# Kernel tuning notes

Hardware: AMD Instinct MI355X
Metric: run time of the kernel (lower is better)

Reference implementation:

```python
import math
import jax, jax.numpy as jnp
import numpy as np


def setup_inputs() -> dict:
    key = jax.random.key(0)
    k1, k2 = jax.random.split(key)
    x = jax.random.normal(k1, (16, 256, 4096), dtype=jnp.float32)          # [B, D, T]
    codebooks = jax.random.normal(k2, (8, 1024, 256), dtype=jnp.float32)   # [n_q, bins, D]
    return {"x": x, "codebooks": codebooks, "sample_rate": 24000}


def _rvq(xt, codebooks):
    """Residual VQ on channels-last input xt: [B, T, D]. codebooks: [n_q, bins, D]."""
    n_q = codebooks.shape[0]
    residual = xt
    quant_out = jnp.zeros_like(xt)
    codes = []
    losses = []
    for i in range(n_q):
        cb = codebooks[i]                                   # [bins, D]
        # squared euclidean distance: ||r||^2 - 2 r.e + ||e||^2  -> [B, T, bins]
        dist = (jnp.sum(residual * residual, axis=-1, keepdims=True)
                - 2.0 * jnp.einsum("btd,kd->btk", residual, cb)
                + jnp.sum(cb * cb, axis=-1))
        idx = jnp.argmin(dist, axis=-1)                     # [B, T]
        q = cb[idx]                                         # gather -> [B, T, D]
        # straight-through estimator
        q_st = residual + jax.lax.stop_gradient(q - residual)
        # commitment loss: mse(stop_grad(quantize), residual)
        losses.append(jnp.mean((jax.lax.stop_gradient(q_st) - residual) ** 2))
        residual = residual - q_st
        quant_out = quant_out + q_st
        codes.append(idx)
    codes = jnp.stack(codes)                                # [n_q, B, T]
    commit_loss = jnp.stack(losses)                         # [n_q]
    return quant_out, codes, commit_loss


def reference(x, codebooks, sample_rate):
    n_q, bins, _ = codebooks.shape
    bw_per_q = math.log2(bins) * sample_rate / 1000.0
    xt = jnp.transpose(x, (0, 2, 1))                        # [B, T, D]
    quant_out, codes, commit_loss = _rvq(xt, codebooks)
    quantized = jnp.transpose(quant_out, (0, 2, 1))         # [B, D, T]
    bw = jnp.asarray(n_q * bw_per_q, dtype=x.dtype)
    return quantized, codes, bw, jnp.mean(commit_loss)
```

## Files before the change

### kernel.cpp

```cpp
#include <hip/hip_runtime.h>

#define B 16
#define D 256
#define T 4096
#define NQ 8
#define BINS 1024
#define EPS 0.008f

#define OFF_C  ((size_t)B * D * T)
#define OFF_BW (OFF_C + (size_t)NQ * B * T)
#define OFF_L  (OFF_BW + 1)

typedef __attribute__((ext_vector_type(8))) short short8v;
typedef __attribute__((ext_vector_type(4))) float float4v;

#define BUF0   0
#define BUF1   16384
#define BUF2   32768
#define RESF   0
#define IDXS   16448
#define FLAGS  16704
#define G1L    16960
#define RSTG   17216
#define REDW   18240
#define REDIW  18272
#define NORMS  49152
#define SMTOT  53248

#define STAGE16(gp, loff) \
  __builtin_amdgcn_global_load_lds( \
      (const __attribute__((address_space(1))) unsigned int*)(gp), \
      (__attribute__((address_space(3))) unsigned int*)(smc + (loff)), 16, 0, 0)

__device__ __forceinline__ unsigned short f2bf(float f) {
    unsigned u = __float_as_uint(f);
    unsigned r = (u + 0x7fffu + ((u >> 16) & 1u)) >> 16;
    return (unsigned short)r;
}
__device__ __forceinline__ float bf2f(unsigned short h) {
    return __uint_as_float(((unsigned)h) << 16);
}

__global__ __launch_bounds__(256) void cbnorm_kernel(const float* __restrict__ cb,
                                                     double* __restrict__ cbn,
                                                     float* __restrict__ cbnf)
{
    const int wave = threadIdx.x >> 6;
    const int lane = threadIdx.x & 63;
    const int bin = blockIdx.x * 4 + wave;
    const float4 v = *(const float4*)&cb[(size_t)bin * D + lane * 4];
    double a = (double)v.x * v.x + (double)v.y * v.y
             + (double)v.z * v.z + (double)v.w * v.w;
    #pragma unroll
    for (int off = 32; off >= 1; off >>= 1)
        a += __shfl_xor(a, off, 64);
    if (lane == 0) { cbn[bin] = a; cbnf[bin] = (float)a; }
}

__global__ __launch_bounds__(256) void prep_bfrag(const float* __restrict__ cb,
                                                  unsigned short* __restrict__ bfh,
                                                  unsigned short* __restrict__ bfl)
{
    const int c = blockIdx.x * 4 + (threadIdx.x >> 6);
    const int lane = threadIdx.x & 63;
    const int q = c >> 9, ntg = (c >> 3) & 63, ks = c & 7;
    const float* src = cb + ((size_t)q * BINS + ntg * 16 + (lane & 15)) * D
                         + ks * 32 + (lane >> 4) * 8;
    short8v h, l;
    #pragma unroll
    for (int j = 0; j < 8; ++j) {
        const float v = src[j];
        const unsigned short hh = f2bf(v);
        h[j] = (short)hh;
        l[j] = (short)f2bf(v - bf2f(hh));
    }
    const size_t off = ((size_t)c * 64 + lane) * 8;
    *(short8v*)(bfh + off) = h;
    *(short8v*)(bfl + off) = l;
}

__global__ __launch_bounds__(256, 3) void rvq_scan(
    const float* __restrict__ rsrc, float* __restrict__ rdst,
    const float* __restrict__ cb,
    const double* __restrict__ cbn, const float* __restrict__ cbnf,
    const unsigned short* __restrict__ bfh, const unsigned short* __restrict__ bfl,
    float* __restrict__ out, double* __restrict__ lpart, int q)
{
    __shared__ __align__(16) char smem[SMTOT];
    char*   smc    = smem;
    float*  resf   = (float*)(smem + RESF);
    int*    idxsL  = (int*)(smem + IDXS);
    int*    flagsL = (int*)(smem + FLAGS);
    float*  g1L    = (float*)(smem + G1L);
    float*  rstage = (float*)(smem + RSTG);
    float*  normsp = (float*)(smem + NORMS);
    double* redw   = (double*)(smem + REDW);
    int*    rediw  = (int*)(smem + REDIW);

    const int tid  = threadIdx.x;
    const int bid  = blockIdx.x;
    const int b    = bid >> 6;
    const int t0   = (bid & 63) * 64;
    const int w    = tid >> 6;
    const int lane = tid & 63;
    const int col  = lane & 15;
    const int rgrp = lane >> 4;
    const int rot  = (bid * 5) & 63;

    const float* rs = rsrc + (size_t)b * D * T + t0;
    float*       rd = rdst + (size_t)b * D * T + t0;

    for (int i = tid; i < BINS; i += 256) normsp[i] = cbnf[q * BINS + i];

    short8v Ah[8], Al[8];
    #pragma unroll 1
    for (int ch = 0; ch < 4; ++ch) {
        #pragma unroll
        for (int it = 0; it < 4; ++it) {
            const int tk4 = (tid & 3) * 4;
            const int d   = it * 64 + (tid >> 2);
            const float4 v = *(const float4*)&rs[(size_t)d * T + ch * 16 + tk4];
            resf[(tk4 + 0) * 257 + d] = v.x;
            resf[(tk4 + 1) * 257 + d] = v.y;
            resf[(tk4 + 2) * 257 + d] = v.z;
            resf[(tk4 + 3) * 257 + d] = v.w;
        }
        __syncthreads();
        if (w == ch) {
            #pragma unroll
            for (int ks = 0; ks < 8; ++ks) {
                short8v h, l;
                #pragma unroll
                for (int j = 0; j < 8; ++j) {
                    const float v = resf[col * 257 + ks * 32 + rgrp * 8 + j];
                    const unsigned short hh = f2bf(v);
                    h[j] = (short)hh;
                    l[j] = (short)f2bf(v - bf2f(hh));
                }
                Ah[ks] = h; Al[ks] = l;
            }
        }
        __syncthreads();
    }

    const int plane = w >> 1, part = w & 1;
    const unsigned short* sbase = plane ? bfl : bfh;

    #pragma unroll
    for (int pnt = 0; pnt < 2; ++pnt) {
        const int ntg = (pnt + rot) & 63;
        const unsigned short* srcp =
            sbase + ((size_t)q * 512 + ntg * 8 + part * 4) * 512 + lane * 8;
        const int dstb = pnt * 16384 + plane * 8192 + part * 4096;
        #pragma unroll
        for (int i = 0; i < 4; ++i) STAGE16(srcp + i * 512, dstb + i * 1024);
    }

    float bv1[4], bv2[4]; int bi1[4];
    #pragma unroll
    for (int s = 0; s < 4; ++s) { bv1[s] = 3.4e38f; bv2[s] = 3.4e38f; bi1[s] = 0; }

    int bufc = 0;
    #pragma unroll 1
    for (int nt = 0; nt < 64; ++nt) {
        if (nt < 63) { asm volatile("s_waitcnt vmcnt(4)" ::: "memory"); }
        else         { asm volatile("s_waitcnt vmcnt(0)" ::: "memory"); }
        __builtin_amdgcn_s_barrier();
        asm volatile("" ::: "memory");

        if (nt < 62) {
            const int ntg = (nt + 2 + rot) & 63;
            int p2 = bufc + 2; if (p2 >= 3) p2 -= 3;
            const unsigned short* srcp =
                sbase + ((size_t)q * 512 + ntg * 8 + part * 4) * 512 + lane * 8;
            const int dstb = p2 * 16384 + plane * 8192 + part * 4096;
            #pragma unroll
            for (int i = 0; i < 4; ++i) STAGE16(srcp + i * 512, dstb + i * 1024);
        }
        asm volatile("" ::: "memory");

        const int ntr = (nt + rot) & 63;
        const char* bb = smc + bufc * 16384;
        const float qn = normsp[ntr * 16 + col];

        float4v a0 = {0,0,0,0}, a1 = {0,0,0,0}, a2 = {0,0,0,0}, a3 = {0,0,0,0};
        __builtin_amdgcn_s_setprio(1);
        #pragma unroll
        for (int ks = 0; ks < 8; ++ks) {
            const short8v Bh = *(const short8v*)(bb + ks * 1024 + lane * 16);
            const short8v Bl = *(const short8v*)(bb + 8192 + ks * 1024 + lane * 16);
            float4v& c = (ks & 3) == 0 ? a0 : ((ks & 3) == 1 ? a1 : ((ks & 3) == 2 ? a2 : a3));
            c = __builtin_amdgcn_mfma_f32_16x16x32_bf16(Al[ks], Bh, c, 0, 0, 0);
            c = __builtin_amdgcn_mfma_f32_16x16x32_bf16(Ah[ks], Bl, c, 0, 0, 0);
            c = __builtin_amdgcn_mfma_f32_16x16x32_bf16(Ah[ks], Bh, c, 0, 0, 0);
        }
        __builtin_amdgcn_s_setprio(0);

        const int binb = ntr * 16 + col;
        #pragma unroll
        for (int r = 0; r < 4; ++r) {
            const float s0 = fmaf(-2.0f, (a0[r] + a1[r]) + (a2[r] + a3[r]), qn);
            if (s0 < bv1[r]) { bv2[r] = bv1[r]; bv1[r] = s0; bi1[r] = binb; }
            else if (s0 < bv2[r]) bv2[r] = s0;
        }

        bufc = (bufc == 2) ? 0 : bufc + 1;
    }
    __syncthreads();

    #pragma unroll
    for (int off = 1; off <= 8; off <<= 1) {
        #pragma unroll
        for (int sl = 0; sl < 4; ++sl) {
            const float ov1 = __shfl_xor(bv1[sl], off, 64);
            const float ov2 = __shfl_xor(bv2[sl], off, 64);
            const int   oi  = __shfl_xor(bi1[sl], off, 64);
            if (ov1 < bv1[sl] || (ov1 == bv1[sl] && oi < bi1[sl])) {
                bv2[sl] = fminf(bv1[sl], ov2); bv1[sl] = ov1; bi1[sl] = oi;
            } else {
                bv2[sl] = fminf(bv2[sl], ov1);
            }
        }
    }
    if (col == 0) {
        #pragma unroll
        for (int r = 0; r < 4; ++r) {
            const int tk = w * 16 + rgrp * 4 + r;
            idxsL[tk]  = bi1[r];
            g1L[tk]    = bv1[r];
            flagsL[tk] = (bv2[r] - bv1[r] < EPS) ? 1 : 0;
        }
    }
    __syncthreads();

    const float* cbq = cb + (size_t)q * BINS * D;
    #pragma unroll 1
    for (int tk2 = 0; tk2 < 64; ++tk2) {
        if (!flagsL[tk2]) continue;
        rstage[tid] = rs[(size_t)tid * T + tk2];
        __syncthreads();
        const float thr = g1L[tk2] + 0.0065f;
        double bb2 = 1e300; int bbi = 0x7fffffff;
        #pragma unroll 1
        for (int jj = 0; jj < 4; ++jj) {
            const int bin = tid + 256 * jj;
            const float* crow = cbq + (size_t)bin * D;
            float f0 = 0.f, f1 = 0.f, f2 = 0.f, f3 = 0.f;
            for (int d = 0; d < D; d += 4) {
                const float4 rv = *(const float4*)&rstage[d];
                const float4 cv = *(const float4*)&crow[d];
                f0 = fmaf(rv.x, cv.x, f0); f1 = fmaf(rv.y, cv.y, f1);
                f2 = fmaf(rv.z, cv.z, f2); f3 = fmaf(rv.w, cv.w, f3);
            }
            const float sf = fmaf(-2.0f, (f0 + f1) + (f2 + f3), normsp[bin]);
            if (sf <= thr) {
                double a = 0.0;
                for (int d = 0; d < D; d += 4) {
                    const float4 rv = *(const float4*)&rstage[d];
                    const float4 cv = *(const float4*)&crow[d];
                    a = fma((double)rv.x, (double)cv.x, a);
                    a = fma((double)rv.y, (double)cv.y, a);
                    a = fma((double)rv.z, (double)cv.z, a);
                    a = fma((double)rv.w, (double)cv.w, a);
                }
                const double s = fma(-2.0, a, cbn[q * BINS + bin]);
                if (s < bb2) { bb2 = s; bbi = bin; }
            }
        }
        #pragma unroll
        for (int off = 32; off >= 1; off >>= 1) {
            const double ov = __shfl_xor(bb2, off, 64);
            const int   oi  = __shfl_xor(bbi, off, 64);
            if (ov < bb2 || (ov == bb2 && oi < bbi)) { bb2 = ov; bbi = oi; }
        }
        if (lane == 0) { redw[w] = bb2; rediw[w] = bbi; }
        __syncthreads();
        if (tid == 0) {
            double mv = redw[0]; int mi = rediw[0];
            #pragma unroll
            for (int wv = 1; wv < 4; ++wv) {
                const double ov = redw[wv]; const int oi = rediw[wv];
                if (ov < mv || (ov == mv && oi < mi)) { mv = ov; mi = oi; }
            }
            idxsL[tk2] = mi;
        }
        __syncthreads();
    }

    if (tid < 64)
        out[OFF_C + (size_t)q * B * T + (size_t)b * T + t0 + tid] = (float)idxsL[tid];

    float* rows = resf;
    double lacc = 0.0;
    #pragma unroll 1
    for (int g = 0; g < 4; ++g) {
        __syncthreads();
        {
            const int j = tid >> 4, c = tid & 15;
            const float* crow = cbq + (size_t)idxsL[g * 16 + j] * D + c * 16;
            #pragma unroll
            for (int k2 = 0; k2 < 4; ++k2) {
                const float4 v = *(const float4*)(crow + k2 * 4);
                *(float4*)&rows[j * 257 + c * 16 + k2 * 4] = v;
            }
        }
        __syncthreads();
        #pragma unroll
        for (int it = 0; it < 4; ++it) {
            const int tk4 = (tid & 3) * 4;
            const int dd_ = it * 64 + (tid >> 2);
            const int tk  = g * 16 + tk4;
            const float4 rv = *(const float4*)&rs[(size_t)dd_ * T + tk];
            const float c0 = rows[(tk4 + 0) * 257 + dd_];
            const float c1 = rows[(tk4 + 1) * 257 + dd_];
            const float c2 = rows[(tk4 + 2) * 257 + dd_];
            const float c3 = rows[(tk4 + 3) * 257 + dd_];
            float4 od;
            float e, qst, dv;
            e = c0 - rv.x; qst = rv.x + e; dv = qst - rv.x;
            lacc = fma((double)dv, (double)dv, lacc); od.x = rv.x - qst;
            e = c1 - rv.y; qst = rv.y + e; dv = qst - rv.y;
            lacc = fma((double)dv, (double)dv, lacc); od.y = rv.y - qst;
            e = c2 - rv.z; qst = rv.z + e; dv = qst - rv.z;
            lacc = fma((double)dv, (double)dv, lacc); od.z = rv.z - qst;
            e = c3 - rv.w; qst = rv.w + e; dv = qst - rv.w;
            lacc = fma((double)dv, (double)dv, lacc); od.w = rv.w - qst;
            *(float4*)&rd[(size_t)dd_ * T + tk] = od;
        }
    }

    #pragma unroll
    for (int off = 32; off >= 1; off >>= 1)
        lacc += __shfl_xor(lacc, off, 64);
    __syncthreads();
    if (lane == 0) redw[w] = lacc;
    __syncthreads();
    if (tid == 0)
        lpart[(size_t)q * 1024 + bid] = (redw[0] + redw[1]) + (redw[2] + redw[3]);
}

__global__ __launch_bounds__(256) void final_sub(const float* __restrict__ x,
                                                 float* __restrict__ o)
{
    const size_t i = ((size_t)blockIdx.x * 256 + threadIdx.x) * 4;
    const float4v xv = __builtin_nontemporal_load((const float4v*)(x + i));
    const float4v ov = __builtin_nontemporal_load((const float4v*)(o + i));
    const float4v r = xv - ov;
    __builtin_nontemporal_store(r, (float4v*)(o + i));
}

#define OTOK 32
#define ORS 260
__global__ __launch_bounds__(256, 3) void rvq_main_old(
    const float* __restrict__ x, const float* __restrict__ cb,
    const double* __restrict__ cbn, const float* __restrict__ cbnf,
    float* __restrict__ out, double* __restrict__ lpart)
{
    __shared__ float  res[OTOK][ORS];
    __shared__ float  bv1s[OTOK][16];
    __shared__ float  bv2s[OTOK][16];
    __shared__ int    bi1s[OTOK][16];
    __shared__ int    idxs[OTOK];
    __shared__ int    flags[OTOK];
    __shared__ double fbv[256];
    __shared__ int    fbi[256];

    const int tid = threadIdx.x;
    const int bid = blockIdx.x;
    const int b  = bid >> 7;
    const int t0 = (bid & 127) * OTOK;

    const float* xb = x + (size_t)b * D * T + t0;
    #pragma unroll
    for (int it = 0; it < 32; ++it) {
        const int d  = it * 8 + (tid >> 5);
        const int tk = tid & 31;
        res[tk][d] = xb[(size_t)d * T + tk];
    }
    __syncthreads();

    float qreg[32];
    #pragma unroll
    for (int i = 0; i < 32; ++i) qreg[i] = 0.0f;

    const int tg = tid & 15;
    const int bg = tid >> 4;
    const int tku = tid >> 3;
    const int d0u = (tid & 7) * 32;
    double lacc = 0.0;

    for (int q = 0; q < NQ; ++q) {
        const float*  cbq = cb   + (size_t)q * BINS * D;
        const float*  cnf = cbnf + (size_t)q * BINS;
        const double* cnd = cbn  + (size_t)q * BINS;

        float bvA = 3.4e38f, bvA2 = 3.4e38f;  int biA = 0;
        float bvB = 3.4e38f, bvB2 = 3.4e38f;  int biB = 0;

        for (int iter = 0; iter < 8; ++iter) {
            const int binbase = iter * 128 + bg * 8;
            float a0[8], a1[8];
            #pragma unroll
            for (int j = 0; j < 8; ++j) { a0[j] = 0.0f; a1[j] = 0.0f; }
            for (int d = 0; d < D; d += 4) {
                const float4 r0 = *(const float4*)&res[tg][d];
                const float4 r1 = *(const float4*)&res[tg + 16][d];
                #pragma unroll
                for (int j = 0; j < 8; ++j) {
                    const float4 c = *(const float4*)&cbq[(size_t)(binbase + j) * D + d];
                    a0[j] = fmaf(r0.x, c.x, a0[j]); a0[j] = fmaf(r0.y, c.y, a0[j]);
                    a0[j] = fmaf(r0.z, c.z, a0[j]); a0[j] = fmaf(r0.w, c.w, a0[j]);
                    a1[j] = fmaf(r1.x, c.x, a1[j]); a1[j] = fmaf(r1.y, c.y, a1[j]);
                    a1[j] = fmaf(r1.z, c.z, a1[j]); a1[j] = fmaf(r1.w, c.w, a1[j]);
                }
            }
            #pragma unroll
            for (int j = 0; j < 8; ++j) {
                const int bin = binbase + j;
                const float qn = cnf[bin];
                const float s0 = fmaf(-2.0f, a0[j], qn);
                const float s1 = fmaf(-2.0f, a1[j], qn);
                if (s0 < bvA) { bvA2 = bvA; bvA = s0; biA = bin; }
                else if (s0 < bvA2) { bvA2 = s0; }
                if (s1 < bvB) { bvB2 = bvB; bvB = s1; biB = bin; }
                else if (s1 < bvB2) { bvB2 = s1; }
            }
        }
        bv1s[tg][bg]      = bvA;  bv2s[tg][bg]      = bvA2;  bi1s[tg][bg]      = biA;
        bv1s[tg + 16][bg] = bvB;  bv2s[tg + 16][bg] = bvB2;  bi1s[tg + 16][bg] = biB;
        __syncthreads();

        if (tid < OTOK) {
            float g1 = bv1s[tid][0], g2 = bv2s[tid][0];
            int   gi = bi1s[tid][0];
            #pragma unroll
            for (int g = 1; g < 16; ++g) {
                const float v1 = bv1s[tid][g];
                const float v2 = bv2s[tid][g];
                const int   i1 = bi1s[tid][g];
                if (v1 < g1 || (v1 == g1 && i1 < gi)) { g2 = fminf(g1, v2); g1 = v1; gi = i1; }
                else g2 = fminf(g2, v1);
            }
            idxs[tid]  = gi;
            flags[tid] = (g2 - g1 < 0.02f) ? 1 : 0;
        }
        __syncthreads();

        for (int tok = 0; tok < OTOK; ++tok) {
            if (!flags[tok]) continue;
            double bb = 1e300; int bbi = 0;
            #pragma unroll
            for (int jj = 0; jj < 4; ++jj) {
                const int bin = tid + 256 * jj;
                const float* crow = cbq + (size_t)bin * D;
                double a = 0.0;
                for (int d = 0; d < D; d += 4) {
                    const float4 r = *(const float4*)&res[tok][d];
                    const float4 c = *(const float4*)&crow[d];
                    a = fma((double)r.x, (double)c.x, a);
                    a = fma((double)r.y, (double)c.y, a);
                    a = fma((double)r.z, (double)c.z, a);
                    a = fma((double)r.w, (double)c.w, a);
                }
                const double s = fma(-2.0, a, cnd[bin]);
                if (s < bb) { bb = s; bbi = bin; }
            }
            fbv[tid] = bb; fbi[tid] = bbi;
            __syncthreads();
            for (int s2 = 128; s2 >= 1; s2 >>= 1) {
                if (tid < s2) {
                    const double ov = fbv[tid + s2]; const int oi = fbi[tid + s2];
                    const double mv = fbv[tid];      const int mi = fbi[tid];
                    if (ov < mv || (ov == mv && oi < mi)) { fbv[tid] = ov; fbi[tid] = oi; }
                }
                __syncthreads();
            }
            if (tid == 0) idxs[tok] = fbi[0];
            __syncthreads();
        }

        if (tid < OTOK)
            out[OFF_C + (size_t)q * B * T + (size_t)b * T + t0 + tid] = (float)idxs[tid];

        const float* crow = cbq + (size_t)idxs[tku] * D;
        #pragma unroll
        for (int i = 0; i < 8; ++i) {
            const int d = d0u + i * 4;
            const float4 qv = *(const float4*)&crow[d];
            float4 r = *(float4*)&res[tku][d];
            float e, qst, dd;
            e = qv.x - r.x; qst = r.x + e; dd = qst - r.x;
            lacc = fma((double)dd, (double)dd, lacc); qreg[i*4+0] += qst; r.x = r.x - qst;
            e = qv.y - r.y; qst = r.y + e; dd = qst - r.y;
            lacc = fma((double)dd, (double)dd, lacc); qreg[i*4+1] += qst; r.y = r.y - qst;
            e = qv.z - r.z; qst = r.z + e; dd = qst - r.z;
            lacc = fma((double)dd, (double)dd, lacc); qreg[i*4+2] += qst; r.z = r.z - qst;
            e = qv.w - r.w; qst = r.w + e; dd = qst - r.w;
            lacc = fma((double)dd, (double)dd, lacc); qreg[i*4+3] += qst; r.w = r.w - qst;
            *(float4*)&res[tku][d] = r;
        }
        __syncthreads();
    }

    #pragma unroll
    for (int i = 0; i < 8; ++i)
        *(float4*)&res[tku][d0u + i * 4] = *(float4*)&qreg[i * 4];
    __syncthreads();
    #pragma unroll
    for (int it = 0; it < 32; ++it) {
        const int d  = it * 8 + (tid >> 5);
        const int tk = tid & 31;
        out[(size_t)b * D * T + (size_t)d * T + t0 + tk] = res[tk][d];
    }

    fbv[tid] = lacc;
    __syncthreads();
    for (int s2 = 128; s2 >= 1; s2 >>= 1) {
        if (tid < s2) fbv[tid] += fbv[tid + s2];
        __syncthreads();
    }
    if (tid == 0) lpart[bid] = fbv[0];
}

__global__ __launch_bounds__(256) void finalize_kernel(
    const double* __restrict__ lpart, int nblk,
    const int* __restrict__ srp, float* __restrict__ out)
{
    __shared__ double sh[256];
    double a = 0.0;
    for (int i = threadIdx.x; i < nblk; i += 256) a += lpart[i];
    sh[threadIdx.x] = a;
    __syncthreads();
    for (int s = 128; s >= 1; s >>= 1) {
        if (threadIdx.x < s) sh[threadIdx.x] += sh[threadIdx.x + s];
        __syncthreads();
    }
    if (threadIdx.x == 0) {
        out[OFF_L]  = (float)(sh[0] / ((double)NQ * B * T * D));
        out[OFF_BW] = (float)((double)NQ * 10.0 * (double)srp[0] / 1000.0);
    }
}

extern "C" void kernel_launch(void* const* d_in, const int* in_sizes, int n_in,
                              void* d_out, int out_size, void* d_ws, size_t ws_size,
                              hipStream_t stream)
{
    const float* x  = (const float*)d_in[0];
    const float* cb = (const float*)d_in[1];
    const int*   sr = (const int*)d_in[2];
    float* out = (float*)d_out;

    double* cbn   = (double*)d_ws;
    float*  cbnf  = (float*)((char*)d_ws + 65536);
    double* lpart = (double*)((char*)d_ws + 98304);
    unsigned short* bfh = (unsigned short*)((char*)d_ws + 163840);
    unsigned short* bfl = (unsigned short*)((char*)d_ws + 4358144);

    hipLaunchKernelGGL(cbnorm_kernel, dim3(NQ * BINS / 4), dim3(256), 0, stream, cb, cbn, cbnf);

    if (ws_size >= (size_t)8552448) {
        hipLaunchKernelGGL(prep_bfrag, dim3(1024), dim3(256), 0, stream, cb, bfh, bfl);
        float* resb = out;
        for (int q = 0; q < NQ; ++q) {
            hipLaunchKernelGGL(rvq_scan, dim3(B * (T / 64)), dim3(256), 0, stream,
                               (q == 0 ? x : (const float*)resb), resb, cb, cbn, cbnf,
                               bfh, bfl, out, lpart, q);
        }
        hipLaunchKernelGGL(final_sub, dim3((B * D * T) / 1024), dim3(256), 0, stream, x, resb);
        hipLaunchKernelGGL(finalize_kernel, dim3(1), dim3(256), 0, stream,
                           lpart, NQ * 1024, sr, out);
    } else {
        hipLaunchKernelGGL(rvq_main_old, dim3(B * (T / OTOK)), dim3(256), 0, stream,
                           x, cb, cbn, cbnf, out, lpart);
        hipLaunchKernelGGL(finalize_kernel, dim3(1), dim3(256), 0, stream,
                           lpart, B * (T / OTOK), sr, out);
    }
}
```

Measured before the change: 1.663 ms.

## Load codebook fragments directly from global memory instead of LDS triple buffering

Removes the async global-to-LDS triple-buffered staging of the bf16 hi/lo codebook tiles and the per-tile barrier. Each wave now loads its B fragments straight from global (L2-resident) memory into registers. This shrinks shared memory enough to raise the launch-bounds occupancy hint from 3 to 4 blocks per CU. The cost is that every wave redundantly fetches the same codebook tile through the cache hierarchy, and load latency is no longer hidden by explicit prefetch.

```diff
diff --git a/kernel.cpp b/kernel.cpp
--- a/kernel.cpp
+++ b/kernel.cpp
@@ -14,9 +14,6 @@
 typedef __attribute__((ext_vector_type(8))) short short8v;
 typedef __attribute__((ext_vector_type(4))) float float4v;
 
-#define BUF0   0
-#define BUF1   16384
-#define BUF2   32768
 #define RESF   0
 #define IDXS   16448
 #define FLAGS  16704
@@ -24,13 +21,8 @@
 #define RSTG   17216
 #define REDW   18240
 #define REDIW  18272
-#define NORMS  49152
-#define SMTOT  53248
-
-#define STAGE16(gp, loff) \
-  __builtin_amdgcn_global_load_lds( \
-      (const __attribute__((address_space(1))) unsigned int*)(gp), \
-      (__attribute__((address_space(3))) unsigned int*)(smc + (loff)), 16, 0, 0)
+#define NORMS  18304
+#define SMTOT  22400
 
 __device__ __forceinline__ unsigned short f2bf(float f) {
     unsigned u = __float_as_uint(f);
@@ -79,7 +71,7 @@
     *(short8v*)(bfl + off) = l;
 }
 
-__global__ __launch_bounds__(256, 3) void rvq_scan(
+__global__ __launch_bounds__(256, 4) void rvq_scan(
     const float* __restrict__ rsrc, float* __restrict__ rdst,
     const float* __restrict__ cb,
     const double* __restrict__ cbn, const float* __restrict__ cbnf,
@@ -87,7 +79,6 @@
     float* __restrict__ out, double* __restrict__ lpart, int q)
 {
     __shared__ __align__(16) char smem[SMTOT];
-    char*   smc    = smem;
     float*  resf   = (float*)(smem + RESF);
     int*    idxsL  = (int*)(smem + IDXS);
     int*    flagsL = (int*)(smem + FLAGS);
@@ -143,58 +134,40 @@
         __syncthreads();
     }
 
-    const int plane = w >> 1, part = w & 1;
-    const unsigned short* sbase = plane ? bfl : bfh;
-
-    #pragma unroll
-    for (int pnt = 0; pnt < 2; ++pnt) {
-        const int ntg = (pnt + rot) & 63;
-        const unsigned short* srcp =
-            sbase + ((size_t)q * 512 + ntg * 8 + part * 4) * 512 + lane * 8;
-        const int dstb = pnt * 16384 + plane * 8192 + part * 4096;
-        #pragma unroll
-        for (int i = 0; i < 4; ++i) STAGE16(srcp + i * 512, dstb + i * 1024);
-    }
-
     float bv1[4], bv2[4]; int bi1[4];
     #pragma unroll
     for (int s = 0; s < 4; ++s) { bv1[s] = 3.4e38f; bv2[s] = 3.4e38f; bi1[s] = 0; }
 
-    int bufc = 0;
+    const unsigned short* bqh = bfh + (size_t)q * 512 * 512 + lane * 8;
+    const unsigned short* bql = bfl + (size_t)q * 512 * 512 + lane * 8;
+
     #pragma unroll 1
     for (int nt = 0; nt < 64; ++nt) {
-        if (nt < 63) { asm volatile("s_waitcnt vmcnt(4)" ::: "memory"); }
-        else         { asm volatile("s_waitcnt vmcnt(0)" ::: "memory"); }
-        __builtin_amdgcn_s_barrier();
-        asm volatile("" ::: "memory");
-
-        if (nt < 62) {
-            const int ntg = (nt + 2 + rot) & 63;
-            int p2 = bufc + 2; if (p2 >= 3) p2 -= 3;
-            const unsigned short* srcp =
-                sbase + ((size_t)q * 512 + ntg * 8 + part * 4) * 512 + lane * 8;
-            const int dstb = p2 * 16384 + plane * 8192 + part * 4096;
-            #pragma unroll
-            for (int i = 0; i < 4; ++i) STAGE16(srcp + i * 512, dstb + i * 1024);
-        }
-        asm volatile("" ::: "memory");
-
         const int ntr = (nt + rot) & 63;
-        const char* bb = smc + bufc * 16384;
+        const unsigned short* ph = bqh + (size_t)ntr * 4096;
+        const unsigned short* pl = bql + (size_t)ntr * 4096;
         const float qn = normsp[ntr * 16 + col];
 
         float4v a0 = {0,0,0,0}, a1 = {0,0,0,0}, a2 = {0,0,0,0}, a3 = {0,0,0,0};
-        __builtin_amdgcn_s_setprio(1);
-        #pragma unroll
-        for (int ks = 0; ks < 8; ++ks) {
-            const short8v Bh = *(const short8v*)(bb + ks * 1024 + lane * 16);
-            const short8v Bl = *(const short8v*)(bb + 8192 + ks * 1024 + lane * 16);
-            float4v& c = (ks & 3) == 0 ? a0 : ((ks & 3) == 1 ? a1 : ((ks & 3) == 2 ? a2 : a3));
-            c = __builtin_amdgcn_mfma_f32_16x16x32_bf16(Al[ks], Bh, c, 0, 0, 0);
-            c = __builtin_amdgcn_mfma_f32_16x16x32_bf16(Ah[ks], Bl, c, 0, 0, 0);
-            c = __builtin_amdgcn_mfma_f32_16x16x32_bf16(Ah[ks], Bh, c, 0, 0, 0);
-        }
-        __builtin_amdgcn_s_setprio(0);
+
+        #define KS2(K0, C0, C1) { \
+            const short8v h0 = *(const short8v*)(ph + (K0) * 512); \
+            const short8v l0 = *(const short8v*)(pl + (K0) * 512); \
+            const short8v h1 = *(const short8v*)(ph + ((K0) + 1) * 512); \
+            const short8v l1 = *(const short8v*)(pl + ((K0) + 1) * 512); \
+            __builtin_amdgcn_s_setprio(1); \
+            C0 = __builtin_amdgcn_mfma_f32_16x16x32_bf16(Al[(K0)],     h0, C0, 0, 0, 0); \
+            C0 = __builtin_amdgcn_mfma_f32_16x16x32_bf16(Ah[(K0)],     l0, C0, 0, 0, 0); \
+            C0 = __builtin_amdgcn_mfma_f32_16x16x32_bf16(Ah[(K0)],     h0, C0, 0, 0, 0); \
+            C1 = __builtin_amdgcn_mfma_f32_16x16x32_bf16(Al[(K0) + 1], h1, C1, 0, 0, 0); \
+            C1 = __builtin_amdgcn_mfma_f32_16x16x32_bf16(Ah[(K0) + 1], l1, C1, 0, 0, 0); \
+            C1 = __builtin_amdgcn_mfma_f32_16x16x32_bf16(Ah[(K0) + 1], h1, C1, 0, 0, 0); \
+            __builtin_amdgcn_s_setprio(0); }
+        KS2(0, a0, a1)
+        KS2(2, a2, a3)
+        KS2(4, a0, a1)
+        KS2(6, a2, a3)
+        #undef KS2
 
         const int binb = ntr * 16 + col;
         #pragma unroll
@@ -203,10 +176,7 @@
             if (s0 < bv1[r]) { bv2[r] = bv1[r]; bv1[r] = s0; bi1[r] = binb; }
             else if (s0 < bv2[r]) bv2[r] = s0;
         }
-
-        bufc = (bufc == 2) ? 0 : bufc + 1;
-    }
-    __syncthreads();
+    }
 
     #pragma unroll
     for (int off = 1; off <= 8; off <<= 1) {
```

Result: slower. 1.806 ms (+8.6%).
